# Performance work log

Measured on AMD Instinct MI355X. Metric: run time of the kernel, lower is better.

Reference implementation:

```python
import jax, jax.numpy as jnp
import numpy as np

K_H = 17
K_W = 17
WIN = K_H * K_W  # 289, odd -> lower median == middle element


def setup_inputs() -> dict:
    key = jax.random.key(0)
    x = jax.random.normal(key, (1, 4, 256, 256), dtype=jnp.float32)
    return {"x": x}


def reference(x):
    # same-padding for kernel (1, 17, 17), stride (1, 1, 1):
    # pad_d = 0; pad_h = pad_w = 16 -> (8, 8) each side (matches torch code)
    ph = (K_H - 1) // 2
    pw = (K_W - 1) // 2
    xp = jnp.pad(x, ((0, 0), (0, 0), (ph, K_H - 1 - ph), (pw, K_W - 1 - pw)),
                 mode='constant', constant_values=0.0)
    B, D, H, W = x.shape
    # gather the 17x17 window per output pixel (k_d = 1 so no depth window)
    windows = jnp.stack(
        [xp[:, :, dy:dy + H, dx:dx + W] for dy in range(K_H) for dx in range(K_W)],
        axis=-1)  # [B, D, H, W, 289]
    med = jnp.sort(windows, axis=-1)[..., WIN // 2]
    return med
```

## Files before the change

kernel.cpp:

```cpp
#include <hip/hip_runtime.h>


#define RAD 8
#define KW 17
#define TILE 8
#define IN_W (TILE + 2 * RAD)
#define LDSW 25
#define MEDRANK 144

__global__ __launch_bounds__(256, 3)
void median17_kernel(const float* __restrict__ x, float* __restrict__ out) {
    __shared__ float tile[IN_W * LDSW];

    const int tid = threadIdx.x;
    const int bid = blockIdx.x;
    const int c   = bid >> 10;
    const int t   = bid & 1023;
    const int oy  = (t >> 5) * TILE;
    const int ox  = (t & 31) * TILE;
    const float* xc = x + c * (256 * 256);

    for (int i = tid; i < IN_W * IN_W; i += 256) {
        int r   = i / IN_W;
        int col = i - r * IN_W;
        int gy  = oy - RAD + r;
        int gx  = ox - RAD + col;
        float v = 0.0f;
        if ((unsigned)gy < 256u && (unsigned)gx < 256u) v = xc[gy * 256 + gx];
        tile[r * LDSW + col] = v;
    }
    __syncthreads();

    const int j  = tid & 3;
    const int g  = tid >> 2;
    const int py = g >> 3;
    const int px = g & 7;

    const float FINF = __builtin_inff();

    float w[73];
    {
        int dx = 5 * j;
        int a  = (py + 4 * j) * LDSW + px + dx;
#pragma unroll
        for (int k = 0; k < 73; ++k) {
            bool ok  = (k < 70) || (j < 3);
            float v  = tile[ok ? a : 0];
            w[k]     = ok ? v : FINF;
            bool wrap = (dx == 16);
            a  += wrap ? (LDSW - 16) : 1;
            dx  = wrap ? 0 : dx + 1;
        }
    }

    int cn[4] = {0, 0, 0, 0};
    int ce[4] = {0, 0, 0, 0};
#pragma unroll
    for (int k = 0; k < 73; ++k) {
        cn[k & 3] += (w[k] < 0.0f) ? 1 : 0;
        ce[k & 3] += (w[k] == 0.0f) ? 1 : 0;
    }
    int c0 = (cn[0] + cn[1]) + (cn[2] + cn[3]);
    int cz = (ce[0] + ce[1]) + (ce[2] + ce[3]);
    c0 += __shfl_xor(c0, 1); c0 += __shfl_xor(c0, 2);
    cz += __shfl_xor(cz, 1); cz += __shfl_xor(cz, 2);

    float med;
    if (c0 <= MEDRANK && MEDRANK < c0 + cz) {
        med = 0.0f;
    } else {
        float lo, hi; int lc, hc;
        if (c0 > MEDRANK) { lo = -8.0f; lc = 0;  hi = 0.0f; hc = c0;  }
        else              { lo = 0.0f;  lc = c0; hi = 8.0f; hc = 289; }

        for (int it = 0; it < 30; ++it) {
            if (hc - lc <= 2) break;
            float mid;
            if (it == 0)                       mid = (c0 > MEDRANK) ? -0.175f : 0.175f;
            else if (lo > 0.0f && hi >= 8.0f)  mid = fminf(lo + lo, 0.5f * (lo + hi));
            else if (hi < 0.0f && lo <= -8.0f) mid = fmaxf(hi + hi, 0.5f * (lo + hi));
            else                               mid = 0.5f * (lo + hi);
            if (!(mid > lo && mid < hi)) break;

            int q[4] = {0, 0, 0, 0};
#pragma unroll
            for (int k = 0; k < 73; ++k) q[k & 3] += (w[k] < mid) ? 1 : 0;
            int cnt = (q[0] + q[1]) + (q[2] + q[3]);
            cnt += __shfl_xor(cnt, 1);
            cnt += __shfl_xor(cnt, 2);

            if (cnt <= MEDRANK) { lo = mid; lc = cnt; }
            else                { hi = mid; hc = cnt; }
        }

        int rk = MEDRANK - lc;
        float q0[4], q1[4];
#pragma unroll
        for (int m = 0; m < 4; ++m) { q0[m] = FINF; q1[m] = FINF; }
#pragma unroll
        for (int k = 0; k < 73; ++k) {
            const int m = k & 3;
            float v   = w[k];
            bool  in  = (v >= lo) & (v < hi);
            float xv  = in ? v : FINF;
            float t0  = fminf(q0[m], xv);
            q1[m] = fminf(q1[m], fmaxf(q0[m], xv));
            q0[m] = t0;
        }
        float u0 = fminf(q0[0], q0[1]);
        float u1 = fminf(fminf(q1[0], q1[1]), fmaxf(q0[0], q0[1]));
        float v0 = fminf(q0[2], q0[3]);
        float v1 = fminf(fminf(q1[2], q1[3]), fmaxf(q0[2], q0[3]));
        float s0 = fminf(u0, v0);
        float s1 = fminf(fminf(u1, v1), fmaxf(u0, v0));
        float r0 = __shfl_xor(s0, 1), r1 = __shfl_xor(s1, 1);
        float n0 = fminf(s0, r0);
        float n1 = fminf(fminf(s1, r1), fmaxf(s0, r0));
        s0 = n0; s1 = n1;
        r0 = __shfl_xor(s0, 2); r1 = __shfl_xor(s1, 2);
        n0 = fminf(s0, r0);
        n1 = fminf(fminf(s1, r1), fmaxf(s0, r0));
        s0 = n0; s1 = n1;

        med = (rk == 0) ? s0 : s1;
    }

    if ((tid & 3) == 0) {
        out[c * 65536 + (oy + py) * 256 + (ox + px)] = med;
    }
}

extern "C" void kernel_launch(void* const* d_in, const int* in_sizes, int n_in,
                              void* d_out, int out_size, void* d_ws, size_t ws_size,
                              hipStream_t stream) {
    const float* x = (const float*)d_in[0];
    float* out = (float*)d_out;
    median17_kernel<<<dim3(4096), dim3(256), 0, stream>>>(x, out);
}
```

Before: 118.0 us.

## Split each window across 8 lanes and use interpolated bisection for median search

Each output pixel's 289-element window is now spread over 8 lanes (37 values each) instead of 4 (73 each). The tile shrinks to 8x4 outputs and the grid doubles. This cuts per-thread registers, so occupancy can rise to 4 blocks per CU. The first bisection pivot now comes from a normal-distribution guess based on the negative count, and later steps alternate between interpolation and halving, with open-ended bounds handled by doubling. The cost is an extra shuffle stage per reduction, more LDS halo reloads per output, and a pivot heuristic tuned to Gaussian-like inputs.

```diff
diff --git a/kernel.cpp b/kernel.cpp
--- a/kernel.cpp
+++ b/kernel.cpp
@@ -1,28 +1,30 @@
 #include <hip/hip_runtime.h>
+#include <math.h>
 
 
 #define RAD 8
-#define KW 17
-#define TILE 8
-#define IN_W (TILE + 2 * RAD)
+#define TW 8
+#define TH 4
+#define PW (TW + 2 * RAD)
+#define PH (TH + 2 * RAD)
 #define LDSW 25
 #define MEDRANK 144
 
-__global__ __launch_bounds__(256, 3)
+__global__ __launch_bounds__(256, 4)
 void median17_kernel(const float* __restrict__ x, float* __restrict__ out) {
-    __shared__ float tile[IN_W * LDSW];
+    __shared__ float tile[PH * LDSW];
 
     const int tid = threadIdx.x;
     const int bid = blockIdx.x;
-    const int c   = bid >> 10;
-    const int t   = bid & 1023;
-    const int oy  = (t >> 5) * TILE;
-    const int ox  = (t & 31) * TILE;
-    const float* xc = x + c * (256 * 256);
+    const int c  = bid >> 11;
+    const int t  = bid & 2047;
+    const int oy = (t >> 5) * TH;
+    const int ox = (t & 31) * TW;
+    const float* xc = x + c * 65536;
 
-    for (int i = tid; i < IN_W * IN_W; i += 256) {
-        int r   = i / IN_W;
-        int col = i - r * IN_W;
+    for (int i = tid; i < PH * PW; i += 256) {
+        int r   = i / PW;
+        int col = i - r * PW;
         int gy  = oy - RAD + r;
         int gx  = ox - RAD + col;
         float v = 0.0f;
@@ -31,102 +33,117 @@
     }
     __syncthreads();
 
-    const int j  = tid & 3;
-    const int g  = tid >> 2;
+    const int j  = tid & 7;
+    const int g  = tid >> 3;
     const int py = g >> 3;
     const int px = g & 7;
 
     const float FINF = __builtin_inff();
 
-    float w[73];
+    float w[37];
     {
-        int dx = 5 * j;
-        int a  = (py + 4 * j) * LDSW + px + dx;
+        const int f0  = 37 * j;
+        const int dy0 = f0 / 17;
+        int dx = f0 - dy0 * 17;
+        int a  = (py + dy0) * LDSW + px + dx;
 #pragma unroll
-        for (int k = 0; k < 73; ++k) {
-            bool ok  = (k < 70) || (j < 3);
-            float v  = tile[ok ? a : 0];
-            w[k]     = ok ? v : FINF;
+        for (int k = 0; k < 37; ++k) {
+            bool ok   = (k < 30) || (j < 7);
+            float v   = tile[ok ? a : 0];
+            w[k]      = ok ? v : FINF;
             bool wrap = (dx == 16);
             a  += wrap ? (LDSW - 16) : 1;
             dx  = wrap ? 0 : dx + 1;
         }
     }
 
-    int cn[4] = {0, 0, 0, 0};
-    int ce[4] = {0, 0, 0, 0};
+    int cn = 0, ce = 0;
 #pragma unroll
-    for (int k = 0; k < 73; ++k) {
-        cn[k & 3] += (w[k] < 0.0f) ? 1 : 0;
-        ce[k & 3] += (w[k] == 0.0f) ? 1 : 0;
+    for (int k = 0; k < 37; ++k) {
+        cn += (w[k] < 0.0f) ? 1 : 0;
+        ce += (w[k] == 0.0f) ? 1 : 0;
     }
-    int c0 = (cn[0] + cn[1]) + (cn[2] + cn[3]);
-    int cz = (ce[0] + ce[1]) + (ce[2] + ce[3]);
-    c0 += __shfl_xor(c0, 1); c0 += __shfl_xor(c0, 2);
-    cz += __shfl_xor(cz, 1); cz += __shfl_xor(cz, 2);
+    int pk = cn | (ce << 16);
+    pk += __shfl_xor(pk, 1);
+    pk += __shfl_xor(pk, 2);
+    pk += __shfl_xor(pk, 4);
+    const int c0 = pk & 0xffff;
+    const int cz = pk >> 16;
 
     float med;
     if (c0 <= MEDRANK && MEDRANK < c0 + cz) {
         med = 0.0f;
     } else {
         float lo, hi; int lc, hc;
-        if (c0 > MEDRANK) { lo = -8.0f; lc = 0;  hi = 0.0f; hc = c0;  }
-        else              { lo = 0.0f;  lc = c0; hi = 8.0f; hc = 289; }
+        if (c0 > MEDRANK) { lo = -FINF; lc = 0;  hi = 0.0f; hc = c0;  }
+        else              { lo = 0.0f;  lc = c0; hi = FINF; hc = 289; }
 
-        for (int it = 0; it < 30; ++it) {
+        for (int it = 0; it < 100; ++it) {
             if (hc - lc <= 2) break;
             float mid;
-            if (it == 0)                       mid = (c0 > MEDRANK) ? -0.175f : 0.175f;
-            else if (lo > 0.0f && hi >= 8.0f)  mid = fminf(lo + lo, 0.5f * (lo + hi));
-            else if (hi < 0.0f && lo <= -8.0f) mid = fmaxf(hi + hi, 0.5f * (lo + hi));
-            else                               mid = 0.5f * (lo + hi);
+            if (it == 0) {
+                mid = 2.5066283f * (0.5f - (float)c0 * (1.0f / 289.0f));
+            } else if (hi == FINF) {
+                mid = fminf(2.0f * lo, 3.0e38f);
+            } else if (lo == -FINF) {
+                mid = fmaxf(2.0f * hi, -3.0e38f);
+            } else if (it & 1) {
+                mid = 0.5f * (lo + hi);
+            } else {
+                float wd   = hi - lo;
+                float frac = (float)(144 - lc) + 0.5f;
+                mid = lo + wd * (frac / (float)(hc - lc));
+                mid = fminf(fmaxf(mid, lo + 0.03125f * wd), hi - 0.03125f * wd);
+            }
             if (!(mid > lo && mid < hi)) break;
 
-            int q[4] = {0, 0, 0, 0};
+            int q = 0;
 #pragma unroll
-            for (int k = 0; k < 73; ++k) q[k & 3] += (w[k] < mid) ? 1 : 0;
-            int cnt = (q[0] + q[1]) + (q[2] + q[3]);
-            cnt += __shfl_xor(cnt, 1);
-            cnt += __shfl_xor(cnt, 2);
+            for (int k = 0; k < 37; ++k) q += (w[k] < mid) ? 1 : 0;
+            q += __shfl_xor(q, 1);
+            q += __shfl_xor(q, 2);
+            q += __shfl_xor(q, 4);
 
-            if (cnt <= MEDRANK) { lo = mid; lc = cnt; }
-            else                { hi = mid; hc = cnt; }
+            if (q <= MEDRANK) { lo = mid; lc = q; }
+            else              { hi = mid; hc = q; }
         }
 
-        int rk = MEDRANK - lc;
-        float q0[4], q1[4];
+        const int rk = MEDRANK - lc;
+        float q0a = FINF, q1a = FINF, q0b = FINF, q1b = FINF;
 #pragma unroll
-        for (int m = 0; m < 4; ++m) { q0[m] = FINF; q1[m] = FINF; }
+        for (int k = 0; k < 37; k += 2) {
+            {
+                float v  = w[k];
+                bool in  = (v >= lo) & (v < hi);
+                float xv = in ? v : FINF;
+                float t0 = fminf(q0a, xv);
+                q1a = fminf(q1a, fmaxf(q0a, xv));
+                q0a = t0;
+            }
+            if (k + 1 < 37) {
+                float v  = w[k + 1];
+                bool in  = (v >= lo) & (v < hi);
+                float xv = in ? v : FINF;
+                float t0 = fminf(q0b, xv);
+                q1b = fminf(q1b, fmaxf(q0b, xv));
+                q0b = t0;
+            }
+        }
+        float s0 = fminf(q0a, q0b);
+        float s1 = fminf(fminf(q1a, q1b), fmaxf(q0a, q0b));
 #pragma unroll
-        for (int k = 0; k < 73; ++k) {
-            const int m = k & 3;
-            float v   = w[k];
-            bool  in  = (v >= lo) & (v < hi);
-            float xv  = in ? v : FINF;
-            float t0  = fminf(q0[m], xv);
-            q1[m] = fminf(q1[m], fmaxf(q0[m], xv));
-            q0[m] = t0;
+        for (int d = 1; d <= 4; d <<= 1) {
+            float r0 = __shfl_xor(s0, d);
+            float r1 = __shfl_xor(s1, d);
+            float n0 = fminf(s0, r0);
+            float n1 = fminf(fminf(s1, r1), fmaxf(s0, r0));
+            s0 = n0; s1 = n1;
         }
-        float u0 = fminf(q0[0], q0[1]);
-        float u1 = fminf(fminf(q1[0], q1[1]), fmaxf(q0[0], q0[1]));
-        float v0 = fminf(q0[2], q0[3]);
-        float v1 = fminf(fminf(q1[2], q1[3]), fmaxf(q0[2], q0[3]));
-        float s0 = fminf(u0, v0);
-        float s1 = fminf(fminf(u1, v1), fmaxf(u0, v0));
-        float r0 = __shfl_xor(s0, 1), r1 = __shfl_xor(s1, 1);
-        float n0 = fminf(s0, r0);
-        float n1 = fminf(fminf(s1, r1), fmaxf(s0, r0));
-        s0 = n0; s1 = n1;
-        r0 = __shfl_xor(s0, 2); r1 = __shfl_xor(s1, 2);
-        n0 = fminf(s0, r0);
-        n1 = fminf(fminf(s1, r1), fmaxf(s0, r0));
-        s0 = n0; s1 = n1;
-
         med = (rk == 0) ? s0 : s1;
     }
 
-    if ((tid & 3) == 0) {
-        out[c * 65536 + (oy + py) * 256 + (ox + px)] = med;
+    if (j == 0) {
+        out[c * 65536 + (oy + py) * 256 + ox + px] = med;
     }
 }
 
@@ -135,5 +152,5 @@
                               hipStream_t stream) {
     const float* x = (const float*)d_in[0];
     float* out = (float*)d_out;
-    median17_kernel<<<dim3(4096), dim3(256), 0, stream>>>(x, out);
+    median17_kernel<<<dim3(8192), dim3(256), 0, stream>>>(x, out);
 }
```

Result: slower. 122.6 us (+3.9%).
